# Kernel optimization log

Measured on AMD Instinct MI355X. Metric: run time of the kernel, lower is better.

## Reference

```python
import jax, jax.numpy as jnp
import numpy as np

N = 100000        # num_nodes
E = 3200000       # num_edges
IN_C = 256        # in_channels (feature dim)
OUT_C = 128       # out_channels (embedding dim)
KAPPA = 0.95


def proj_norm_inf(W, kappa):
    """Row-wise projection of W onto the l-inf operator-norm ball of radius kappa:
    rows whose l1 norm exceeds kappa are projected (abs values onto the simplex
    of radius kappa via sort, signs restored). Matches projection_norm_inf."""
    a = jnp.abs(W)
    s = jnp.sign(W)
    rowsum = a.sum(axis=-1)                      # [rows]
    n = W.shape[-1]
    u = jnp.sort(a, axis=-1)[:, ::-1]            # descending
    css = jnp.cumsum(u, axis=-1) - kappa
    ind = jnp.arange(1, n + 1, dtype=W.dtype)
    cond = (u - css / ind) > 0                   # prefix-true pattern
    rho = jnp.sum(cond, axis=-1)                 # number of active coords (>=1 when rowsum>kappa)
    rho_safe = jnp.maximum(rho, 1)
    theta = jnp.take_along_axis(css, (rho_safe - 1)[:, None], axis=-1)[:, 0] / rho_safe.astype(W.dtype)
    w_proj = jnp.maximum(a - theta[:, None], 0.0) * s
    return jnp.where((rowsum > kappa)[:, None], w_proj, W)


def gcn_conv(x, W, src, dst, num_nodes):
    """PyG GCNConv (bias=False, normalize=True, add_self_loops=True):
    out = D^{-1/2} (A + I) D^{-1/2} (x @ W.T)"""
    loop = jnp.arange(num_nodes, dtype=src.dtype)
    src_f = jnp.concatenate([src, loop])
    dst_f = jnp.concatenate([dst, loop])
    ones = jnp.ones(src_f.shape[0], dtype=x.dtype)
    deg = jax.ops.segment_sum(ones, dst_f, num_segments=num_nodes)   # [N]
    dinv = jnp.where(deg > 0, jax.lax.rsqrt(jnp.maximum(deg, 1.0)), 0.0)
    norm = dinv[src_f] * dinv[dst_f]                                 # [E+N]
    h = x @ W.T                                                      # [N, OUT_C]
    msg = h[src_f] * norm[:, None]                                   # gather + scale
    return jax.ops.segment_sum(msg, dst_f, num_segments=num_nodes)   # scatter-add


def setup_inputs() -> dict:
    key = jax.random.key(0)
    k1, k2, k3, k4, k5 = jax.random.split(key, 5)
    features = jax.random.normal(k1, (N, IN_C), dtype=jnp.float32)
    edge_index = jax.random.randint(k2, (2, E), 0, N, dtype=jnp.int32)
    embeddings = 0.01 * jax.random.uniform(k3, (N, OUT_C), dtype=jnp.float32)
    # xavier_uniform-ish init for weights
    lim_c = float(np.sqrt(6.0 / (OUT_C + OUT_C)))
    lim_m = float(np.sqrt(6.0 / (IN_C + OUT_C)))
    W_conv = jax.random.uniform(k4, (OUT_C, OUT_C), dtype=jnp.float32, minval=-lim_c, maxval=lim_c)
    W_mlp = jax.random.uniform(k5, (OUT_C, IN_C), dtype=jnp.float32, minval=-lim_m, maxval=lim_m)
    return {"features": features, "edge_index": edge_index, "embeddings": embeddings,
            "W_conv": W_conv, "W_mlp": W_mlp}


def reference(features, edge_index, embeddings, W_conv, W_mlp):
    # SoftIGNN.forward: project conv weight, then one IGNN layer:
    # x = relu(GCNConv(embeddings, edge_index) + Linear(features))
    W_p = proj_norm_inf(W_conv, KAPPA)
    src, dst = edge_index[0], edge_index[1]
    agg = gcn_conv(embeddings, W_p, src, dst, N)     # [N, OUT_C]
    x = agg + features @ W_mlp.T                     # [N, OUT_C]
    return jax.nn.relu(x)
```

## Files before the change

### kernel.cpp

```cpp
#include <hip/hip_runtime.h>

#define KAPPA 0.95f

typedef __attribute__((ext_vector_type(8))) short short8;
typedef __attribute__((ext_vector_type(4))) float f32x4;
typedef __attribute__((ext_vector_type(2))) float f32x2;

static __device__ inline unsigned short f2bf(float f) {
    unsigned int u = __float_as_uint(f);
    unsigned int rounding = 0x7fffu + ((u >> 16) & 1u);
    u += rounding;
    return (unsigned short)(u >> 16);
}
static __device__ inline unsigned int pack2bf(float x, float y) {
    return (unsigned int)f2bf(x) | ((unsigned int)f2bf(y) << 16);
}

#define H_SCALE 4096.0f

__global__ __launch_bounds__(128) void proj_kernel(const float* __restrict__ W,
                                                   unsigned short* __restrict__ Wp_bf) {
    const int r = blockIdx.x;
    const int tid = threadIdx.x;
    __shared__ float s[128];
    __shared__ float c[128];
    __shared__ int rho_s;

    const float w = W[r * 128 + tid];
    const float a = fabsf(w);
    s[tid] = a;
    if (tid == 0) rho_s = 0;
    __syncthreads();

    for (int k = 2; k <= 128; k <<= 1) {
        for (int j = k >> 1; j > 0; j >>= 1) {
            int ixj = tid ^ j;
            if (ixj > tid) {
                bool up = ((tid & k) == 0);
                float x = s[tid], y = s[ixj];
                if ((x > y) == up) { s[tid] = y; s[ixj] = x; }
            }
            __syncthreads();
        }
    }

    const float u = s[127 - tid];
    c[tid] = u;
    __syncthreads();
    for (int off = 1; off < 128; off <<= 1) {
        float add = (tid >= off) ? c[tid - off] : 0.f;
        __syncthreads();
        c[tid] += add;
        __syncthreads();
    }
    const float rowsum = c[127];
    const float css = c[tid] - KAPPA;
    if (u - css / (float)(tid + 1) > 0.f) atomicAdd(&rho_s, 1);
    __syncthreads();

    float out = w;
    if (rowsum > KAPPA) {
        int rho = max(rho_s, 1);
        float theta = (c[rho - 1] - KAPPA) / (float)rho;
        float m = fmaxf(a - theta, 0.f);
        out = (w > 0.f) ? m : ((w < 0.f) ? -m : 0.f);
    }
    Wp_bf[r * 128 + tid] = f2bf(out);
}

__global__ void convw_kernel(const float* __restrict__ Wm, unsigned short* __restrict__ Wbf,
                             int n) {
    int i = blockIdx.x * blockDim.x + threadIdx.x;
    if (i < n) Wbf[i] = f2bf(Wm[i]);
}

__global__ __launch_bounds__(256) void rhist_kernel(const int* __restrict__ dst,
                                                    int* __restrict__ l2c, int E, unsigned N,
                                                    int chunk) {
    __shared__ int hist[512];
    const int b = blockIdx.x;
    const int i0 = b * chunk;
    const int i1 = min(i0 + chunk, E);
    for (int t = threadIdx.x; t < 512; t += 256) hist[t] = 0;
    __syncthreads();
    for (int i = i0 + threadIdx.x; i < i1; i += 256) {
        unsigned g = ((unsigned)dst[i] * 512u) / N;
        atomicAdd(&hist[g], 1);
    }
    __syncthreads();
    for (int t = threadIdx.x; t < 512; t += 256) l2c[(t << 9) | b] = hist[t];
}

__global__ __launch_bounds__(256) void rsum_kernel(const int* __restrict__ l2c,
                                                   int* __restrict__ R) {
    __shared__ int tmp[256];
    const int g = blockIdx.x;
    int s = 0;
    for (int j = threadIdx.x; j < 512; j += 256) s += l2c[(g << 9) | j];
    tmp[threadIdx.x] = s;
    __syncthreads();
    for (int off = 128; off > 0; off >>= 1) {
        if (threadIdx.x < off) tmp[threadIdx.x] += tmp[threadIdx.x + off];
        __syncthreads();
    }
    if (threadIdx.x == 0) R[g] = tmp[0];
}

__global__ __launch_bounds__(512) void rscan_kernel(const int* __restrict__ R,
                                                    int* __restrict__ Gbase) {
    __shared__ int tmp[512];
    const int tid = threadIdx.x;
    int v = R[tid];
    tmp[tid] = v;
    __syncthreads();
    int val = v;
    for (int off = 1; off < 512; off <<= 1) {
        int add = (tid >= off) ? tmp[tid - off] : 0;
        __syncthreads();
        val += add;
        tmp[tid] = val;
        __syncthreads();
    }
    Gbase[tid] = val - v;
}

__global__ __launch_bounds__(512) void rowscan_kernel(const int* __restrict__ l2c,
                                                      const int* __restrict__ Gbase,
                                                      int* __restrict__ l2base) {
    __shared__ int tmp[512];
    const int g = blockIdx.x;
    const int tid = threadIdx.x;
    int v = l2c[(g << 9) | tid];
    tmp[tid] = v;
    __syncthreads();
    int val = v;
    for (int off = 1; off < 512; off <<= 1) {
        int add = (tid >= off) ? tmp[tid - off] : 0;
        __syncthreads();
        val += add;
        tmp[tid] = val;
        __syncthreads();
    }
    l2base[(g << 9) | tid] = Gbase[g] + val - v;
}

__global__ __launch_bounds__(256) void rpart_kernel(const int* __restrict__ src,
                                                    const int* __restrict__ dst,
                                                    const int* __restrict__ l2base,
                                                    unsigned* __restrict__ queue2, int E,
                                                    unsigned N, int chunk) {
    __shared__ int base[512];
    const int b = blockIdx.x;
    const int i0 = b * chunk;
    const int i1 = min(i0 + chunk, E);
    for (int t = threadIdx.x; t < 512; t += 256) base[t] = l2base[(t << 9) | b];
    __syncthreads();
    for (int i = i0 + threadIdx.x; i < i1; i += 256) {
        unsigned d = (unsigned)dst[i];
        unsigned s = (unsigned)src[i];
        unsigned g = (d * 512u) / N;
        unsigned v0g = (g * N + 511u) >> 9;
        int p = atomicAdd(&base[g], 1);
        queue2[p] = ((d - v0g) << 24) | s;
    }
}

__global__ __launch_bounds__(1024) void subfill_kernel(const unsigned* __restrict__ queue2,
                                                       const int* __restrict__ Gbase,
                                                       int* __restrict__ csr_src,
                                                       int* __restrict__ counts,
                                                       int* __restrict__ cursor,
                                                       float* __restrict__ dinv, unsigned N,
                                                       int E) {
    __shared__ int cnt[256];
    __shared__ int ofs[256];
    __shared__ int stage[8192];
    const int B = blockIdx.x;
    const int g = (B & 7) * 64 + (B >> 3);
    const int e0 = Gbase[g];
    const int e1 = (g == 511) ? E : Gbase[g + 1];
    const unsigned v0 = ((unsigned)g * N + 511u) >> 9;
    const unsigned v1 = min((((unsigned)g + 1u) * N + 511u) >> 9, N);
    const int nn = (int)(v1 - v0);
    const int tid = threadIdx.x;
    if (tid < 256) cnt[tid] = 0;
    __syncthreads();
    for (int i = e0 + tid; i < e1; i += 1024) atomicAdd(&cnt[queue2[i] >> 24], 1);
    __syncthreads();
    if (tid < 256) ofs[tid] = cnt[tid];
    __syncthreads();
    for (int off = 1; off < 256; off <<= 1) {
        int add = (tid < 256 && tid >= off) ? ofs[tid - off] : 0;
        __syncthreads();
        if (tid < 256) ofs[tid] += add;
        __syncthreads();
    }
    if (tid < nn) {
        int excl = ofs[tid] - cnt[tid];
        counts[v0 + tid] = cnt[tid];
        cursor[v0 + tid] = e0 + excl;
        dinv[v0 + tid] = rsqrtf((float)(cnt[tid] + 1));
    }
    __syncthreads();
    if (tid < 256) ofs[tid] -= cnt[tid];
    __syncthreads();
    for (int i = e0 + tid; i < e1; i += 1024) {
        unsigned raw = queue2[i];
        int p = atomicAdd(&ofs[raw >> 24], 1);
        stage[p] = (int)(raw & 0xFFFFFFu);
    }
    __syncthreads();
    const int tot = e1 - e0;
    for (int t = tid; t < tot; t += 1024) csr_src[e0 + t] = stage[t];
}

template <int KD, int MODE>
__global__ __launch_bounds__(512) void gemm_mfma(const float* __restrict__ X,
                                                 const unsigned short* __restrict__ Wbf,
                                                 const float* __restrict__ dinv,
                                                 const float* ADD,
                                                 unsigned int* __restrict__ out_u32,
                                                 float* out_f, int nrows) {
    __shared__ __align__(16) unsigned short ldsW[128 * KD];
    const int tid = threadIdx.x;
    const int w = tid >> 6;
    const int l = tid & 63;
    const int l16 = l & 15;
    const int kg = l >> 4;
    const unsigned swz = (unsigned)((l16 & 7) << 4);
    const int row0 = blockIdx.x * 128;
    const int row = row0 + w * 16 + l16;
    const int rload = min(row, nrows - 1);
    const float* xrow = X + (size_t)rload * KD + kg * 8;

    {
        const uint4* wsrc = reinterpret_cast<const uint4*>(Wbf);
        char* lb = reinterpret_cast<char*>(ldsW);
        constexpr int NCH = 128 * KD / 8;
#pragma unroll
        for (int i = 0; i < NCH / 512; ++i) {
            int idx = i * 512 + tid;
            int sidx = idx * 8;
            unsigned byte = (unsigned)(sidx * 2);
            byte ^= (unsigned)(((sidx / KD) & 7) << 4);
            *reinterpret_cast<uint4*>(lb + byte) = wsrc[idx];
        }
    }
    __syncthreads();

    f32x4 acc[8];
#pragma unroll
    for (int j = 0; j < 8; ++j) acc[j] = (f32x4)(0.f);

    const char* lbr = reinterpret_cast<const char*>(ldsW);
    constexpr int NT = KD / 32;
#pragma unroll
    for (int t = 0; t < NT; ++t) {
        const float4 v0 = *reinterpret_cast<const float4*>(xrow + t * 32);
        const float4 v1 = *reinterpret_cast<const float4*>(xrow + t * 32 + 4);
        union { uint4 u; short8 s; } cvt;
        cvt.u.x = pack2bf(v0.x, v0.y);
        cvt.u.y = pack2bf(v0.z, v0.w);
        cvt.u.z = pack2bf(v1.x, v1.y);
        cvt.u.w = pack2bf(v1.z, v1.w);
        const short8 a = cvt.s;
#pragma unroll
        for (int ct = 0; ct < 8; ++ct) {
            const int c = ct * 16 + l16;
            unsigned byte = (unsigned)((c * KD + t * 32 + kg * 8) * 2) ^ swz;
            short8 wv = *reinterpret_cast<const short8*>(lbr + byte);
            acc[ct] = __builtin_amdgcn_mfma_f32_16x16x32_bf16(wv, a, acc[ct], 0, 0, 0);
        }
    }

    if (row < nrows) {
        if (MODE == 0) {
            const float dv = dinv[row] * H_SCALE;
#pragma unroll
            for (int ct = 0; ct < 8; ++ct) {
                f32x4 d = acc[ct];
                unsigned lo = __builtin_amdgcn_cvt_pk_fp8_f32(d[0] * dv, d[1] * dv, 0u, false);
                unsigned hi = __builtin_amdgcn_cvt_pk_fp8_f32(d[2] * dv, d[3] * dv, lo, true);
                out_u32[(size_t)row * 32 + ct * 4 + kg] = hi;
            }
        } else {
#pragma unroll
            for (int ct = 0; ct < 8; ++ct) {
                f32x4 d = acc[ct];
                const float4 a =
                    *reinterpret_cast<const float4*>(&ADD[(size_t)row * 128 + ct * 16 + kg * 4]);
                float4 o;
                o.x = fmaxf(d[0] + a.x, 0.f);
                o.y = fmaxf(d[1] + a.y, 0.f);
                o.z = fmaxf(d[2] + a.z, 0.f);
                o.w = fmaxf(d[3] + a.w, 0.f);
                *reinterpret_cast<float4*>(&out_f[(size_t)row * 128 + ct * 16 + kg * 4]) = o;
            }
        }
    }
}

static __device__ inline void unp8v(f32x2* acc, unsigned wv, int off) {
    acc[off + 0] += __builtin_amdgcn_cvt_pk_f32_fp8(wv, false);
    acc[off + 1] += __builtin_amdgcn_cvt_pk_f32_fp8(wv, true);
}
static __device__ inline void unp16(f32x2* acc, uint4 val) {
    unp8v(acc, val.x, 0);
    unp8v(acc, val.y, 2);
    unp8v(acc, val.z, 4);
    unp8v(acc, val.w, 6);
}

__global__ __launch_bounds__(256) void agg_kernel(const uint4* __restrict__ h8,
                                                  const int* __restrict__ csr_src,
                                                  const int* __restrict__ cursor,
                                                  const int* __restrict__ counts,
                                                  const float* __restrict__ dinv,
                                                  float* __restrict__ agg, int n) {
    int v = blockIdx.x * 4 + (threadIdx.x >> 6);
    if (v >= n) return;
    const int lane = threadIdx.x & 63;
    const int eg = lane >> 3;
    const int c = lane & 7;
    const int cnt = counts[v];
    const int start = cursor[v];

    f32x2 acc[8];
#pragma unroll
    for (int j = 0; j < 8; ++j) acc[j] = (f32x2)(0.f);

    int i0 = (eg < cnt) ? csr_src[start + eg] : -1;
    int i1 = (8 + eg < cnt) ? csr_src[start + 8 + eg] : -1;
    for (int base = 0; base < cnt; base += 16) {
        int s0 = i0, s1 = i1;
        int n0 = base + 16 + eg;
        int n1 = base + 24 + eg;
        i0 = (n0 < cnt) ? csr_src[start + n0] : -1;
        i1 = (n1 < cnt) ? csr_src[start + n1] : -1;
        uint4 va, vb;
        if (s0 >= 0) va = h8[(size_t)s0 * 8 + c];
        if (s1 >= 0) vb = h8[(size_t)s1 * 8 + c];
        if (s0 >= 0) unp16(acc, va);
        if (s1 >= 0) unp16(acc, vb);
    }
    if (eg == 0) {
        uint4 val = h8[(size_t)v * 8 + c];
        unp16(acc, val);
    }
#pragma unroll
    for (int j = 0; j < 8; ++j) {
#pragma unroll
        for (int k = 0; k < 2; ++k) {
            acc[j][k] += __shfl_xor(acc[j][k], 8);
            acc[j][k] += __shfl_xor(acc[j][k], 16);
            acc[j][k] += __shfl_xor(acc[j][k], 32);
        }
    }
    if (eg == 0) {
        const float dv = dinv[v] * (1.0f / H_SCALE);
#pragma unroll
        for (int k = 0; k < 4; ++k) {
            float4 o = {acc[2 * k][0] * dv, acc[2 * k][1] * dv, acc[2 * k + 1][0] * dv,
                        acc[2 * k + 1][1] * dv};
            *reinterpret_cast<float4*>(&agg[(size_t)v * 128 + c * 16 + k * 4]) = o;
        }
    }
}

extern "C" void kernel_launch(void* const* d_in, const int* in_sizes, int n_in,
                              void* d_out, int out_size, void* d_ws, size_t ws_size,
                              hipStream_t stream) {
    const float* features = (const float*)d_in[0];
    const int*   edge     = (const int*)d_in[1];
    const float* emb      = (const float*)d_in[2];
    const float* Wconv    = (const float*)d_in[3];
    const float* Wmlp     = (const float*)d_in[4];
    float* out = (float*)d_out;

    const int N = in_sizes[0] / 256;
    const int E = in_sizes[1] / 2;
    const int* src = edge;
    const int* dst = edge + E;
    const int chunk = (E + 511) / 512;

    char* ws = (char*)d_ws;
    size_t o = 0;
    auto take = [&](size_t b) {
        size_t cur = o;
        o += (b + 255) & ~(size_t)255;
        return cur;
    };
    unsigned short* Wp_bf   = (unsigned short*)(ws + take((size_t)128 * 128 * 2));
    unsigned short* Wm_bf   = (unsigned short*)(ws + take((size_t)128 * 256 * 2));
    int*            counts  = (int*)(ws + take((size_t)N * 4));
    int*            cursor  = (int*)(ws + take((size_t)N * 4));
    float*          dinv    = (float*)(ws + take((size_t)N * 4));
    int*            l2c     = (int*)(ws + take((size_t)512 * 512 * 4));
    int*            l2base  = (int*)(ws + take((size_t)512 * 512 * 4));
    int*            R       = (int*)(ws + take((size_t)512 * 4));
    int*            Gbase   = (int*)(ws + take((size_t)512 * 4));
    int*            csr_src = (int*)(ws + take((size_t)E * 4));
    size_t qbytes = (size_t)E * 4;
    size_t hbytes = (size_t)N * 128;
    char*  qh     = ws + take(qbytes > hbytes ? qbytes : hbytes);
    unsigned*     queue2 = (unsigned*)qh;
    unsigned int* h8     = (unsigned int*)qh;
    (void)ws_size; (void)n_in; (void)out_size;

    hipLaunchKernelGGL(proj_kernel, dim3(128), dim3(128), 0, stream, Wconv, Wp_bf);
    hipLaunchKernelGGL(convw_kernel, dim3((128 * 256 + 255) / 256), dim3(256), 0, stream, Wmlp,
                       Wm_bf, 128 * 256);
    hipLaunchKernelGGL(rhist_kernel, dim3(512), dim3(256), 0, stream, dst, l2c, E, (unsigned)N,
                       chunk);
    hipLaunchKernelGGL(rsum_kernel, dim3(512), dim3(256), 0, stream, l2c, R);
    hipLaunchKernelGGL(rscan_kernel, dim3(1), dim3(512), 0, stream, R, Gbase);
    hipLaunchKernelGGL(rowscan_kernel, dim3(512), dim3(512), 0, stream, l2c, Gbase, l2base);
    hipLaunchKernelGGL(rpart_kernel, dim3(512), dim3(256), 0, stream, src, dst, l2base, queue2, E,
                       (unsigned)N, chunk);
    hipLaunchKernelGGL(subfill_kernel, dim3(512), dim3(1024), 0, stream, queue2, Gbase, csr_src,
                       counts, cursor, dinv, (unsigned)N, E);
    hipLaunchKernelGGL((gemm_mfma<128, 0>), dim3((N + 127) / 128), dim3(512), 0, stream, emb,
                       Wp_bf, dinv, (const float*)nullptr, h8, (float*)nullptr, N);
    hipLaunchKernelGGL(agg_kernel, dim3((N + 3) / 4), dim3(256), 0, stream, (const uint4*)h8,
                       csr_src, cursor, counts, dinv, out, N);
    hipLaunchKernelGGL((gemm_mfma<256, 1>), dim3((N + 127) / 128), dim3(512), 0, stream, features,
                       Wm_bf, (const float*)nullptr, out, (unsigned int*)nullptr, out, N);
}
```

Baseline: 206.4 us.

## Pad per-node CSR lists to 16 with zero-row sentinel and fuse scan kernels

Each node's neighbor list is padded to a multiple of 16 inside a fixed-capacity per-bin region. Padding slots point to an extra zeroed row appended to h8, and stored indices are pre-scaled by 8. This lets the aggregation loop run without bounds checks or predicated loads, and the global bin scan is folded into the row-scan kernel to remove one launch. In exchange the padded entries cost extra gathers of the zero row, every block redoes the 512-entry scan, and a bin that holds more than BIN_CAP padded edges would overflow.

```diff
diff --git a/kernel.cpp b/kernel.cpp
--- a/kernel.cpp
+++ b/kernel.cpp
@@ -17,6 +17,7 @@
 }
 
 #define H_SCALE 4096.0f
+#define BIN_CAP 10240
 
 __global__ __launch_bounds__(128) void proj_kernel(const float* __restrict__ W,
                                                    unsigned short* __restrict__ Wp_bf) {
@@ -106,11 +107,23 @@
     if (threadIdx.x == 0) R[g] = tmp[0];
 }
 
-__global__ __launch_bounds__(512) void rscan_kernel(const int* __restrict__ R,
-                                                    int* __restrict__ Gbase) {
+__global__ __launch_bounds__(512) void rowscan_kernel(const int* __restrict__ l2c,
+                                                      const int* __restrict__ R,
+                                                      int* __restrict__ l2base) {
+    __shared__ int tmpR[512];
     __shared__ int tmp[512];
+    const int g = blockIdx.x;
     const int tid = threadIdx.x;
-    int v = R[tid];
+    tmpR[tid] = R[tid];
+    __syncthreads();
+    for (int off = 1; off < 512; off <<= 1) {
+        int add = (tid >= off) ? tmpR[tid - off] : 0;
+        __syncthreads();
+        tmpR[tid] += add;
+        __syncthreads();
+    }
+    const int gbase = (g == 0) ? 0 : tmpR[g - 1];
+    int v = l2c[(g << 9) | tid];
     tmp[tid] = v;
     __syncthreads();
     int val = v;
@@ -121,27 +134,7 @@
         tmp[tid] = val;
         __syncthreads();
     }
-    Gbase[tid] = val - v;
-}
-
-__global__ __launch_bounds__(512) void rowscan_kernel(const int* __restrict__ l2c,
-                                                      const int* __restrict__ Gbase,
-                                                      int* __restrict__ l2base) {
-    __shared__ int tmp[512];
-    const int g = blockIdx.x;
-    const int tid = threadIdx.x;
-    int v = l2c[(g << 9) | tid];
-    tmp[tid] = v;
-    __syncthreads();
-    int val = v;
-    for (int off = 1; off < 512; off <<= 1) {
-        int add = (tid >= off) ? tmp[tid - off] : 0;
-        __syncthreads();
-        val += add;
-        tmp[tid] = val;
-        __syncthreads();
-    }
-    l2base[(g << 9) | tid] = Gbase[g] + val - v;
+    l2base[(g << 9) | tid] = gbase + val - v;
 }
 
 __global__ __launch_bounds__(256) void rpart_kernel(const int* __restrict__ src,
@@ -166,28 +159,31 @@
 }
 
 __global__ __launch_bounds__(1024) void subfill_kernel(const unsigned* __restrict__ queue2,
-                                                       const int* __restrict__ Gbase,
+                                                       const int* __restrict__ l2base,
                                                        int* __restrict__ csr_src,
                                                        int* __restrict__ counts,
                                                        int* __restrict__ cursor,
-                                                       float* __restrict__ dinv, unsigned N,
+                                                       float* __restrict__ dinv,
+                                                       unsigned* __restrict__ h8z, unsigned N,
                                                        int E) {
     __shared__ int cnt[256];
     __shared__ int ofs[256];
-    __shared__ int stage[8192];
+    __shared__ int stage[BIN_CAP];
     const int B = blockIdx.x;
     const int g = (B & 7) * 64 + (B >> 3);
-    const int e0 = Gbase[g];
-    const int e1 = (g == 511) ? E : Gbase[g + 1];
+    const int e0 = l2base[g << 9];
+    const int e1 = (g == 511) ? E : l2base[(g + 1) << 9];
     const unsigned v0 = ((unsigned)g * N + 511u) >> 9;
     const unsigned v1 = min((((unsigned)g + 1u) * N + 511u) >> 9, N);
     const int nn = (int)(v1 - v0);
     const int tid = threadIdx.x;
+    if (g == 511 && tid < 32) h8z[(size_t)N * 32 + tid] = 0u;
     if (tid < 256) cnt[tid] = 0;
     __syncthreads();
     for (int i = e0 + tid; i < e1; i += 1024) atomicAdd(&cnt[queue2[i] >> 24], 1);
     __syncthreads();
-    if (tid < 256) ofs[tid] = cnt[tid];
+    int cp = 0;
+    if (tid < 256) { cp = (cnt[tid] + 15) & ~15; ofs[tid] = cp; }
     __syncthreads();
     for (int off = 1; off < 256; off <<= 1) {
         int add = (tid < 256 && tid >= off) ? ofs[tid - off] : 0;
@@ -195,23 +191,26 @@
         if (tid < 256) ofs[tid] += add;
         __syncthreads();
     }
+    const int ptot = ofs[255];
     if (tid < nn) {
-        int excl = ofs[tid] - cnt[tid];
+        int pexcl = ofs[tid] - cp;
         counts[v0 + tid] = cnt[tid];
-        cursor[v0 + tid] = e0 + excl;
+        cursor[v0 + tid] = g * BIN_CAP + pexcl;
         dinv[v0 + tid] = rsqrtf((float)(cnt[tid] + 1));
     }
     __syncthreads();
-    if (tid < 256) ofs[tid] -= cnt[tid];
+    if (tid < 256) ofs[tid] -= cp;
+    __syncthreads();
+    const int sent = (int)(N * 8u);
+    for (int t = tid; t < ptot; t += 1024) stage[t] = sent;
     __syncthreads();
     for (int i = e0 + tid; i < e1; i += 1024) {
         unsigned raw = queue2[i];
         int p = atomicAdd(&ofs[raw >> 24], 1);
-        stage[p] = (int)(raw & 0xFFFFFFu);
-    }
-    __syncthreads();
-    const int tot = e1 - e0;
-    for (int t = tid; t < tot; t += 1024) csr_src[e0 + t] = stage[t];
+        stage[p] = (int)((raw & 0xFFFFFFu) << 3);
+    }
+    __syncthreads();
+    for (int t = tid; t < ptot; t += 1024) csr_src[g * BIN_CAP + t] = stage[t];
 }
 
 template <int KD, int MODE>
@@ -324,26 +323,24 @@
     const int c = lane & 7;
     const int cnt = counts[v];
     const int start = cursor[v];
+    const int cnt_pad = (cnt + 15) & ~15;
 
     f32x2 acc[8];
 #pragma unroll
     for (int j = 0; j < 8; ++j) acc[j] = (f32x2)(0.f);
 
-    int i0 = (eg < cnt) ? csr_src[start + eg] : -1;
-    int i1 = (8 + eg < cnt) ? csr_src[start + 8 + eg] : -1;
-    for (int base = 0; base < cnt; base += 16) {
-        int s0 = i0, s1 = i1;
-        int n0 = base + 16 + eg;
-        int n1 = base + 24 + eg;
-        i0 = (n0 < cnt) ? csr_src[start + n0] : -1;
-        i1 = (n1 < cnt) ? csr_src[start + n1] : -1;
-        uint4 va, vb;
-        if (s0 >= 0) va = h8[(size_t)s0 * 8 + c];
-        if (s1 >= 0) vb = h8[(size_t)s1 * 8 + c];
-        if (s0 >= 0) unp16(acc, va);
-        if (s1 >= 0) unp16(acc, vb);
-    }
-    if (eg == 0) {
+    int s0 = csr_src[start + eg];
+    int s1 = csr_src[start + 8 + eg];
+    for (int base = 0; base < cnt_pad; base += 16) {
+        int t0 = s0, t1 = s1;
+        s0 = csr_src[start + base + 16 + eg];
+        s1 = csr_src[start + base + 24 + eg];
+        uint4 va = h8[t0 + c];
+        uint4 vb = h8[t1 + c];
+        unp16(acc, va);
+        unp16(acc, vb);
+    }
+    {
         uint4 val = h8[(size_t)v * 8 + c];
         unp16(acc, val);
     }
@@ -398,10 +395,9 @@
     int*            l2c     = (int*)(ws + take((size_t)512 * 512 * 4));
     int*            l2base  = (int*)(ws + take((size_t)512 * 512 * 4));
     int*            R       = (int*)(ws + take((size_t)512 * 4));
-    int*            Gbase   = (int*)(ws + take((size_t)512 * 4));
-    int*            csr_src = (int*)(ws + take((size_t)E * 4));
+    int*            csr_src = (int*)(ws + take((size_t)512 * BIN_CAP * 4 + 256));
     size_t qbytes = (size_t)E * 4;
-    size_t hbytes = (size_t)N * 128;
+    size_t hbytes = (size_t)(N + 1) * 128;
     char*  qh     = ws + take(qbytes > hbytes ? qbytes : hbytes);
     unsigned*     queue2 = (unsigned*)qh;
     unsigned int* h8     = (unsigned int*)qh;
@@ -413,12 +409,11 @@
     hipLaunchKernelGGL(rhist_kernel, dim3(512), dim3(256), 0, stream, dst, l2c, E, (unsigned)N,
                        chunk);
     hipLaunchKernelGGL(rsum_kernel, dim3(512), dim3(256), 0, stream, l2c, R);
-    hipLaunchKernelGGL(rscan_kernel, dim3(1), dim3(512), 0, stream, R, Gbase);
-    hipLaunchKernelGGL(rowscan_kernel, dim3(512), dim3(512), 0, stream, l2c, Gbase, l2base);
+    hipLaunchKernelGGL(rowscan_kernel, dim3(512), dim3(512), 0, stream, l2c, R, l2base);
     hipLaunchKernelGGL(rpart_kernel, dim3(512), dim3(256), 0, stream, src, dst, l2base, queue2, E,
                        (unsigned)N, chunk);
-    hipLaunchKernelGGL(subfill_kernel, dim3(512), dim3(1024), 0, stream, queue2, Gbase, csr_src,
-                       counts, cursor, dinv, (unsigned)N, E);
+    hipLaunchKernelGGL(subfill_kernel, dim3(512), dim3(1024), 0, stream, queue2, l2base, csr_src,
+                       counts, cursor, dinv, h8, (unsigned)N, E);
     hipLaunchKernelGGL((gemm_mfma<128, 0>), dim3((N + 127) / 128), dim3(512), 0, stream, emb,
                        Wp_bf, dinv, (const float*)nullptr, h8, (float*)nullptr, N);
     hipLaunchKernelGGL(agg_kernel, dim3((N + 3) / 4), dim3(256), 0, stream, (const uint4*)h8,
```

Measured after the change: 208.7 us. Within noise of the previous version (+1.1%).
